# Performance work log

Hardware: AMD Instinct MI355X
Metric: run time of the kernel (lower is better)

The kernel has to match this reference:

```python
import jax, jax.numpy as jnp
import numpy as np

D_MODEL = 1024
NUM_HEADS = 16
D_HEAD = D_MODEL // NUM_HEADS
THETA = 10000.0
B, S = 2, 2048


def setup_inputs() -> dict:
    key = jax.random.key(0)
    ks = jax.random.split(key, 5)
    std = np.sqrt(2.0 / (D_MODEL + D_MODEL))
    x = jax.random.normal(ks[0], (B, S, D_MODEL), dtype=jnp.float32)
    Wq = jax.random.normal(ks[1], (D_MODEL, D_MODEL), dtype=jnp.float32) * std
    Wk = jax.random.normal(ks[2], (D_MODEL, D_MODEL), dtype=jnp.float32) * std
    Wv = jax.random.normal(ks[3], (D_MODEL, D_MODEL), dtype=jnp.float32) * std
    Wo = jax.random.normal(ks[4], (D_MODEL, D_MODEL), dtype=jnp.float32) * std
    token_positions = jnp.arange(S, dtype=jnp.int32)
    return {"x": x, "Wq": Wq, "Wk": Wk, "Wv": Wv, "Wo": Wo,
            "token_positions": token_positions}


def _apply_rope(t, token_positions):
    # t: [B, H, S, d_head]; interleaved (even/odd) RoPE
    dh = t.shape[-1]
    inv_freq = 1.0 / (THETA ** (jnp.arange(0, dh, 2, dtype=jnp.float32) / dh))
    freqs = token_positions.astype(jnp.float32)[:, None] * inv_freq  # [S, dh/2]
    cos = jnp.cos(freqs)  # broadcasts over B, H
    sin = jnp.sin(freqs)
    x1 = t[..., 0::2]
    x2 = t[..., 1::2]
    r1 = x1 * cos - x2 * sin
    r2 = x1 * sin + x2 * cos
    return jnp.stack([r1, r2], axis=-1).reshape(t.shape)


def reference(x, Wq, Wk, Wv, Wo, token_positions):
    b, s, d = x.shape
    h, dh = NUM_HEADS, D_HEAD

    def proj(W):
        y = x @ W.T  # [B, S, D]
        return y.reshape(b, s, h, dh).transpose(0, 2, 1, 3)  # [B, H, S, dh]

    q = _apply_rope(proj(Wq), token_positions)
    k = _apply_rope(proj(Wk), token_positions)
    v = proj(Wv)

    scores = jnp.einsum('bhqd,bhkd->bhqk', q, k) / jnp.sqrt(jnp.float32(dh))
    causal = jnp.tril(jnp.ones((s, s), dtype=bool))
    scores = jnp.where(causal, scores, jnp.float32(-jnp.inf))
    attn = jax.nn.softmax(scores, axis=-1)
    out = jnp.einsum('bhqk,bhkd->bhqd', attn, v)  # [B, H, S, dh]
    out = out.transpose(0, 2, 1, 3).reshape(b, s, d)
    return out @ Wo.T
```

## Files before the change

### kernel.cpp

```cpp
#include <hip/hip_runtime.h>
#include <hip/hip_bf16.h>
#include <math.h>

#define DMODEL 1024
#define NHEAD  16
#define DHEAD  64
#define BATCH  2
#define SEQ    2048
#define MROWS  (BATCH * SEQ)

typedef __attribute__((ext_vector_type(8))) __bf16 bf16x8;
typedef __attribute__((ext_vector_type(4))) float  f32x4;

__device__ __forceinline__ void load16_lds(const ushort* g, ushort* l) {
    __builtin_amdgcn_global_load_lds(
        (const __attribute__((address_space(1))) unsigned int*)g,
        (__attribute__((address_space(3))) unsigned int*)l, 16, 0, 0);
}

__device__ __forceinline__ ushort bf16u(float v) {
    __hip_bfloat16 h = __float2bfloat16(v);
    return *reinterpret_cast<ushort*>(&h);
}

__global__ __launch_bounds__(256)
void cast_f32_bf16(const float* __restrict__ s, ushort* __restrict__ d, int n) {
    const int i = (blockIdx.x * 256 + threadIdx.x) * 8;
    if (i >= n) return;
    const f32x4 a = *reinterpret_cast<const f32x4*>(s + i);
    const f32x4 b = *reinterpret_cast<const f32x4*>(s + i + 4);
    bf16x8 o;
    #pragma unroll
    for (int j = 0; j < 4; j++) { o[j] = (__bf16)a[j]; o[4 + j] = (__bf16)b[j]; }
    *reinterpret_cast<bf16x8*>(d + i) = o;
}

__global__ __launch_bounds__(256)
void cast_w4(const float* __restrict__ w0, const float* __restrict__ w1,
             const float* __restrict__ w2, const float* __restrict__ w3,
             ushort* __restrict__ dst) {
    const float* src = (blockIdx.y == 0) ? w0 : (blockIdx.y == 1) ? w1
                     : (blockIdx.y == 2) ? w2 : w3;
    const int i = (blockIdx.x * 256 + threadIdx.x) * 8;
    const f32x4 a = *reinterpret_cast<const f32x4*>(src + i);
    const f32x4 b = *reinterpret_cast<const f32x4*>(src + i + 4);
    bf16x8 o;
    #pragma unroll
    for (int j = 0; j < 4; j++) { o[j] = (__bf16)a[j]; o[4 + j] = (__bf16)b[j]; }
    *reinterpret_cast<bf16x8*>(dst + (size_t)blockIdx.y * DMODEL * DMODEL + i) = o;
}

__global__ __launch_bounds__(256)
void rope_tab(const int* __restrict__ pos, float2* __restrict__ tab) {
    const int idx = blockIdx.x * 256 + threadIdx.x;
    const int s = idx >> 5;
    const int i = idx & 31;
    const float p = (float)pos[s];
    const float inv = exp2f(-(float)i * 0.41524101186092f);
    float sn, cs;
    sincosf(p * inv, &sn, &cs);
    tab[idx] = make_float2(cs, sn);
}

#define QKV_BARRIER() do { asm volatile("" ::: "memory"); \
                           __builtin_amdgcn_s_barrier(); } while (0)

#define RD4(dst, p_)                                                          \
    _Pragma("unroll")                                                         \
    for (int rr_ = 0; rr_ < 4; rr_++)                                         \
        dst[rr_] = *reinterpret_cast<const bf16x8*>((p_) + rr_ * 512);

#define MFMA_G(AFR, BFR, IOFF)                                                \
    __builtin_amdgcn_s_setprio(1);                                            \
    _Pragma("unroll")                                                         \
    for (int im_ = 0; im_ < 4; im_++)                                         \
        _Pragma("unroll")                                                     \
        for (int jn_ = 0; jn_ < 4; jn_++)                                     \
            acc[(IOFF) + im_][jn_] = __builtin_amdgcn_mfma_f32_16x16x32_bf16( \
                AFR[im_], BFR[jn_], acc[(IOFF) + im_][jn_], 0, 0, 0);         \
    __builtin_amdgcn_s_setprio(0);

__global__ __launch_bounds__(512, 2)
void gemm_qkv(const ushort* __restrict__ A, const ushort* __restrict__ B,
              ushort* __restrict__ C, const float2* __restrict__ tab) {
    __shared__ __align__(16) ushort pool[65536];

    const int orig = blockIdx.y * gridDim.x + blockIdx.x;
    const int xcd  = orig & 7;
    const int ixd  = orig >> 3;
    const int by   = xcd * 2 + (ixd / 12);
    const int bx   = ixd % 12;
    const int m0   = by * 256;
    const int n0   = bx * 256;

    const int tid  = threadIdx.x;
    const int lane = tid & 63;
    const int w    = tid >> 6;
    const int l16  = lane & 15;
    const int quad = lane >> 4;
    const int wm   = (w >> 2) * 128;
    const int wn   = (w & 3) * 64;
    const int chq  = (quad ^ ((l16 & 3) ^ ((l16 & 4) >> 1))) << 3;
    const int srow = tid >> 2;
    const int ssc  = (tid & 3) ^ ((srow & 3) ^ ((srow & 4) >> 1));

    const ushort* gA = A + (size_t)(m0 + srow) * DMODEL + ssc * 8;
    const ushort* gB = B + (size_t)(n0 + srow) * DMODEL + ssc * 8;

    auto stageA = [&](int tt, int ks) {
        const int off = tt * 64 + ks * 32;
        const int lb  = ((tt & 1) << 15) + (ks << 13);
        load16_lds(gA + off,                &pool[lb + tid * 8]);
        load16_lds(gA + 128 * DMODEL + off, &pool[lb + 4096 + tid * 8]);
    };
    auto stageB = [&](int tt, int ks) {
        const int off = tt * 64 + ks * 32;
        const int lb  = ((tt & 1) << 15) + 16384 + (ks << 13);
        load16_lds(gB + off,                &pool[lb + tid * 8]);
        load16_lds(gB + 128 * DMODEL + off, &pool[lb + 4096 + tid * 8]);
    };

    stageA(0, 0); stageB(0, 0);
    stageA(0, 1); stageB(0, 1);
    stageA(1, 0); stageB(1, 0);

    f32x4 acc[8][4];
    #pragma unroll
    for (int i = 0; i < 8; i++)
        #pragma unroll
        for (int j = 0; j < 4; j++) acc[i][j] = (f32x4){0.f, 0.f, 0.f, 0.f};

    asm volatile("s_waitcnt vmcnt(4)" ::: "memory");
    __builtin_amdgcn_s_barrier();

    bf16x8 al[4], ah[4], bc[4], bn[4];

    { const ushort* p = pool + (wm + l16) * 32 + chq;           RD4(al, p); }
    { const ushort* q = pool + 16384 + (wn + l16) * 32 + chq;   RD4(bc, q); }

    #pragma unroll 1
    for (int t = 0; t < 16; t++) {
        const int buf  = (t & 1) << 15;
        const int bufn = buf ^ 32768;
        if (t <= 14) { stageA(t + 1, 1); stageB(t + 1, 1); }
        { const ushort* p = pool + buf + (wm + 64 + l16) * 32 + chq;
          RD4(ah, p); }
        MFMA_G(al, bc, 0);
        { const ushort* p = pool + buf + 8192 + (wm + l16) * 32 + chq;
          RD4(al, p);
          const ushort* q = pool + buf + 16384 + 8192 + (wn + l16) * 32 + chq;
          RD4(bn, q); }
        MFMA_G(ah, bc, 4);
        if (t <= 14) { asm volatile("s_waitcnt vmcnt(4)" ::: "memory"); }
        QKV_BARRIER();
        if (t <= 13) { stageA(t + 2, 0); stageB(t + 2, 0); }
        { const ushort* p = pool + buf + 8192 + (wm + 64 + l16) * 32 + chq;
          RD4(ah, p); }
        MFMA_G(al, bn, 0);
        if (t <= 14) {
            const ushort* p = pool + bufn + (wm + l16) * 32 + chq;
            RD4(al, p);
            const ushort* q = pool + bufn + 16384 + (wn + l16) * 32 + chq;
            RD4(bc, q);
        }
        MFMA_G(ah, bn, 4);
        if (t <= 13)      { asm volatile("s_waitcnt vmcnt(4)" ::: "memory"); }
        else if (t == 14) { asm volatile("s_waitcnt vmcnt(0)" ::: "memory"); }
        QKV_BARRIER();
    }

    const int nbase  = n0 + wn;
    const int tensor = nbase >> 10;
    const int hh     = (nbase & 1023) >> 6;
    if (tensor < 2) {
        ushort* Dt = C + (size_t)tensor * ((size_t)MROWS * DMODEL);
        #pragma unroll
        for (int i = 0; i < 8; i++)
            #pragma unroll
            for (int r = 0; r < 4; r++) {
                const int m  = m0 + wm + i * 16 + quad * 4 + r;
                const int bb = m >> 11;
                const int ss = m & (SEQ - 1);
                const float2* trow = tab + ss * 32;
                #pragma unroll
                for (int j = 0; j < 4; j++) {
                    const int f = j * 16 + l16;
                    const float2 cs = trow[f >> 1];
                    const float val = acc[i][j][r];
                    const float prt = __shfl_xor(val, 1, 64);
                    const float out = (f & 1) ? (prt * cs.y + val * cs.x)
                                              : (val * cs.x - prt * cs.y);
                    Dt[(((size_t)(bb * NHEAD + hh)) * SEQ + ss) * DHEAD + f] =
                        bf16u(out);
                }
            }
    } else {
        ushort* Tw = pool + w * 8192;
        #pragma unroll
        for (int i = 0; i < 8; i++)
            #pragma unroll
            for (int j = 0; j < 4; j++) {
                const int f  = j * 16 + l16;
                const int sx = (f & 7) << 3;
                #pragma unroll
                for (int r = 0; r < 4; r += 2) {
                    const int ml = i * 16 + quad * 4 + r;
                    ushort2 pk;
                    pk.x = bf16u(acc[i][j][r]);
                    pk.y = bf16u(acc[i][j][r + 1]);
                    *reinterpret_cast<ushort2*>(&Tw[f * 128 + (ml ^ sx)]) = pk;
                }
            }
        asm volatile("s_waitcnt lgkmcnt(0)" ::: "memory");
        ushort* Dv = C + 2 * ((size_t)MROWS * DMODEL);
        const int c  = lane & 15;
        const int fb = lane >> 4;
        #pragma unroll
        for (int rr = 0; rr < 16; rr++) {
            const int fl = rr * 4 + fb;
            const uint4 v = *reinterpret_cast<const uint4*>(
                &Tw[fl * 128 + ((c << 3) ^ ((fl & 7) << 3))]);
            *reinterpret_cast<uint4*>(
                &Dv[(size_t)(hh * 64 + fl) * MROWS + m0 + wm + (c << 3)]) = v;
        }
    }
}

__global__ __launch_bounds__(256)
void gemm_out64(const ushort* __restrict__ A, const ushort* __restrict__ B,
                float* __restrict__ C) {
    __shared__ __align__(16) ushort pool[12288];
    ushort* As = pool;
    ushort* Bs = pool + 4096;
    const int tid  = threadIdx.x;
    const int m0   = blockIdx.y * 64;
    const int n0   = blockIdx.x * 128;
    const int lane = tid & 63;
    const int w    = tid >> 6;
    const int l16  = lane & 15;
    const int quad = lane >> 4;
    const int wm   = (w >> 1) * 32;
    const int wn   = (w & 1) * 64;
    const int srow = tid >> 2;
    const int scol = (tid & 3) * 8;

    const int am  = m0 + srow;
    const int abb = am >> 11;
    const int ass = am & (SEQ - 1);
    const size_t abase = ((size_t)(abb * NHEAD)) * SEQ * DHEAD + (size_t)ass * DHEAD;

    f32x4 acc[2][4];
    #pragma unroll
    for (int i = 0; i < 2; i++)
        #pragma unroll
        for (int j = 0; j < 4; j++) acc[i][j] = (f32x4){0.f, 0.f, 0.f, 0.f};

    {
        const int h = scol >> 6, dh = scol & 63;
        load16_lds(A + abase + (size_t)h * SEQ * DHEAD + dh, &As[srow * 32 + scol]);
        #pragma unroll
        for (int half = 0; half < 2; half++) {
            const int row = srow + half * 64;
            load16_lds(B + (size_t)(n0 + row) * DMODEL + scol, &Bs[row * 32 + scol]);
        }
    }

    for (int t = 0; t < 32; t++) {
        const int bf = t & 1;
        __syncthreads();
        if (t + 1 < 32) {
            const int k0 = (t + 1) * 32;
            const int kk = k0 + scol;
            const int h = kk >> 6, dh = kk & 63;
            load16_lds(A + abase + (size_t)h * SEQ * DHEAD + dh,
                       &As[(bf ^ 1) * 2048 + srow * 32 + scol]);
            #pragma unroll
            for (int half = 0; half < 2; half++) {
                const int row = srow + half * 64;
                load16_lds(B + (size_t)(n0 + row) * DMODEL + k0 + scol,
                           &Bs[(bf ^ 1) * 4096 + row * 32 + scol]);
            }
        }
        const int oa = bf * 2048, ob_ = bf * 4096;
        bf16x8 af[2], bfr[4];
        #pragma unroll
        for (int s = 0; s < 2; s++)
            af[s] = *reinterpret_cast<const bf16x8*>(
                &As[oa + (wm + s * 16 + l16) * 32 + quad * 8]);
        #pragma unroll
        for (int s = 0; s < 4; s++)
            bfr[s] = *reinterpret_cast<const bf16x8*>(
                &Bs[ob_ + (wn + s * 16 + l16) * 32 + quad * 8]);
        #pragma unroll
        for (int i = 0; i < 2; i++)
            #pragma unroll
            for (int j = 0; j < 4; j++)
                acc[i][j] = __builtin_amdgcn_mfma_f32_16x16x32_bf16(
                    af[i], bfr[j], acc[i][j], 0, 0, 0);
    }
    #pragma unroll
    for (int i = 0; i < 2; i++)
        #pragma unroll
        for (int r = 0; r < 4; r++) {
            const int m = m0 + wm + i * 16 + quad * 4 + r;
            #pragma unroll
            for (int j = 0; j < 4; j++)
                C[(size_t)m * DMODEL + n0 + wn + j * 16 + l16] = acc[i][j][r];
        }
}

__global__ __launch_bounds__(256)
void attn_mfma6(const ushort* __restrict__ qb, const ushort* __restrict__ kb,
                const ushort* __restrict__ vtg, ushort* __restrict__ ob) {
    __shared__ __align__(16) ushort Ks[2][4096];
    __shared__ __align__(16) ushort Vs[2][4096];
    __shared__ ushort Pb[4][16][72];

    const int bh   = blockIdx.x;
    const int b    = bh >> 4;
    const int h    = bh & 15;
    const int qt   = (gridDim.y - 1) - blockIdx.y;
    const int tid  = threadIdx.x;
    const int w    = tid >> 6;
    const int lane = tid & 63;
    const int l16  = lane & 15;
    const int quad = lane >> 4;
    const size_t base = (size_t)bh * SEQ * DHEAD;

    const int qlo = qt * 64 + w * 16;

    const float SC = 0.125f * 1.44269504088896f;
    bf16x8 qa[2];
    {
        const size_t qo = base + (size_t)(qlo + l16) * DHEAD + quad * 8;
        qa[0] = *reinterpret_cast<const bf16x8*>(qb + qo);
        qa[1] = *reinterpret_cast<const bf16x8*>(qb + qo + 32);
        #pragma unroll
        for (int j = 0; j < 8; j++) {
            qa[0][j] = (__bf16)(SC * (float)qa[0][j]);
            qa[1][j] = (__bf16)(SC * (float)qa[1][j]);
        }
    }

    f32x4 oacc[4];
    #pragma unroll
    for (int s = 0; s < 4; s++) oacc[s] = (f32x4){0.f, 0.f, 0.f, 0.f};
    float l_ = 0.f;

    const int c0 = tid,        r0 = c0 >> 3, g0 = (c0 & 7) ^ (r0 & 7);
    const int c1 = 256 + tid,  r1 = c1 >> 3, g1 = (c1 & 7) ^ (r1 & 7);
    const ushort* kg0 = kb + base + (size_t)r0 * DHEAD + g0 * 8;
    const ushort* kg1 = kb + base + (size_t)r1 * DHEAD + g1 * 8;
    const ushort* vg0 = vtg + (size_t)(h * DHEAD + r0) * MROWS + b * SEQ + g0 * 8;
    const ushort* vg1 = vtg + (size_t)(h * DHEAD + r1) * MROWS + b * SEQ + g1 * 8;

    int koff[2][4];
    #pragma unroll
    for (int half = 0; half < 2; half++)
        #pragma unroll
        for (int sub = 0; sub < 4; sub++)
            koff[half][sub] = (sub * 16 + l16) * 64 +
                              (((half * 4 + quad) ^ (l16 & 7)) * 8);

    load16_lds(kg0, &Ks[0][c0 * 8]);
    load16_lds(kg1, &Ks[0][c1 * 8]);
    load16_lds(vg0, &Vs[0][c0 * 8]);
    load16_lds(vg1, &Vs[0][c1 * 8]);

    const int T = qt + 1;
    for (int t = 0; t < T; t++) {
        const int bf = t & 1;
        __syncthreads();
        if (t + 1 < T) {
            const size_t ko = (size_t)(t + 1) * 64 * DHEAD;
            const int    vo = (t + 1) * 64;
            load16_lds(kg0 + ko, &Ks[bf ^ 1][c0 * 8]);
            load16_lds(kg1 + ko, &Ks[bf ^ 1][c1 * 8]);
            load16_lds(vg0 + vo, &Vs[bf ^ 1][c0 * 8]);
            load16_lds(vg1 + vo, &Vs[bf ^ 1][c1 * 8]);
        }

        const bool diag = (t == qt);
        const int nsub = diag ? (w + 1) : 4;
        const int nhv  = diag ? ((w >> 1) + 1) : 2;

        f32x4 sacc[4];
        #pragma unroll
        for (int s = 0; s < 4; s++) sacc[s] = (f32x4){0.f, 0.f, 0.f, 0.f};
        #pragma unroll
        for (int half = 0; half < 2; half++)
            #pragma unroll
            for (int sub = 0; sub < 4; sub++)
                if (sub < nsub) {
                    const bf16x8 kf = *reinterpret_cast<const bf16x8*>(
                        &Ks[bf][koff[half][sub]]);
                    sacc[sub] = __builtin_amdgcn_mfma_f32_16x16x32_bf16(
                        kf, qa[half], sacc[sub], 0, 0, 0);
                }

        float ev[4][4];
        if (diag) {
            const int thr = qlo + l16 - t * 64;
            #pragma unroll
            for (int sub = 0; sub < 4; sub++)
                #pragma unroll
                for (int r = 0; r < 4; r++) {
                    const float e = (sub * 16 + quad * 4 + r <= thr)
                                        ? exp2f(sacc[sub][r]) : 0.f;
                    ev[sub][r] = e;
                    l_ += e;
                }
        } else {
            #pragma unroll
            for (int sub = 0; sub < 4; sub++)
                #pragma unroll
                for (int r = 0; r < 4; r++) {
                    const float e = exp2f(sacc[sub][r]);
                    ev[sub][r] = e;
                    l_ += e;
                }
        }

        #pragma unroll
        for (int sub = 0; sub < 4; sub++) {
            ushort4 pk;
            pk.x = bf16u(ev[sub][0]); pk.y = bf16u(ev[sub][1]);
            pk.z = bf16u(ev[sub][2]); pk.w = bf16u(ev[sub][3]);
            *reinterpret_cast<ushort4*>(&Pb[w][l16][sub * 16 + quad * 4]) = pk;
        }
        bf16x8 pa[2];
        pa[0] = *reinterpret_cast<const bf16x8*>(&Pb[w][l16][quad * 8]);
        pa[1] = *reinterpret_cast<const bf16x8*>(&Pb[w][l16][32 + quad * 8]);

        #pragma unroll
        for (int hk = 0; hk < 2; hk++) {
            if (hk >= nhv) break;
            #pragma unroll
            for (int sf = 0; sf < 4; sf++) {
                const bf16x8 vf = *reinterpret_cast<const bf16x8*>(
                    &Vs[bf][koff[hk][sf]]);
                oacc[sf] = __builtin_amdgcn_mfma_f32_16x16x32_bf16(
                    pa[hk], vf, oacc[sf], 0, 0, 0);
            }
        }
    }

    l_ += __shfl_xor(l_, 16, 64);
    l_ += __shfl_xor(l_, 32, 64);
    float inv[4];
    #pragma unroll
    for (int r = 0; r < 4; r++) inv[r] = 1.f / __shfl(l_, quad * 4 + r, 64);
    #pragma unroll
    for (int sub = 0; sub < 4; sub++)
        #pragma unroll
        for (int r = 0; r < 4; r++) {
            const int q = qlo + quad * 4 + r;
            ob[base + (size_t)q * DHEAD + sub * 16 + l16] =
                bf16u(oacc[sub][r] * inv[r]);
        }
}

extern "C" void kernel_launch(void* const* d_in, const int* in_sizes, int n_in,
                              void* d_out, int out_size, void* d_ws, size_t ws_size,
                              hipStream_t stream) {
    const float* x  = (const float*)d_in[0];
    const float* Wq = (const float*)d_in[1];
    const float* Wk = (const float*)d_in[2];
    const float* Wv = (const float*)d_in[3];
    const float* Wo = (const float*)d_in[4];
    const int* pos = (const int*)d_in[5];

    const size_t TEN = (size_t)MROWS * DMODEL;
    const size_t WEL = (size_t)DMODEL * DMODEL;
    ushort* xb   = (ushort*)d_ws;
    ushort* Wqkv = xb + TEN;
    ushort* Wob  = Wqkv + 3 * WEL;
    ushort* qb   = Wob + WEL;
    ushort* kb   = qb + TEN;
    ushort* vtb  = kb + TEN;
    ushort* ob   = vtb + TEN;
    float2* tab  = (float2*)(ob + TEN);

    dim3 blk(256);
    rope_tab<<<(SEQ * 32) / 256, blk, 0, stream>>>(pos, tab);
    cast_f32_bf16<<<TEN / (8 * 256), blk, 0, stream>>>(x, xb, (int)TEN);
    dim3 gcw(WEL / (8 * 256), 4);
    cast_w4<<<gcw, blk, 0, stream>>>(Wq, Wk, Wv, Wo, Wqkv);

    dim3 gqkv(3 * DMODEL / 256, MROWS / 256);
    gemm_qkv<<<gqkv, dim3(512), 0, stream>>>(xb, Wqkv, qb, tab);

    dim3 gattn(BATCH * NHEAD, SEQ / 64);
    attn_mfma6<<<gattn, blk, 0, stream>>>(qb, kb, vtb, ob);

    dim3 gout(DMODEL / 128, MROWS / 64);
    gemm_out64<<<gout, blk, 0, stream>>>(ob, Wob, (float*)d_out);
}
```

Before: 181.5 us.

## Merge cast kernels and rewrite output GEMM with 128x128 tiles and pipelining

Result: faster. 177.9 us (-2.0%).

```diff
diff --git a/kernel.cpp b/kernel.cpp
--- a/kernel.cpp
+++ b/kernel.cpp
@@ -24,30 +24,29 @@
 }
 
 __global__ __launch_bounds__(256)
-void cast_f32_bf16(const float* __restrict__ s, ushort* __restrict__ d, int n) {
-    const int i = (blockIdx.x * 256 + threadIdx.x) * 8;
-    if (i >= n) return;
-    const f32x4 a = *reinterpret_cast<const f32x4*>(s + i);
-    const f32x4 b = *reinterpret_cast<const f32x4*>(s + i + 4);
+void cast_all(const float* __restrict__ x,  const float* __restrict__ w0,
+              const float* __restrict__ w1, const float* __restrict__ w2,
+              const float* __restrict__ w3, ushort* __restrict__ xb,
+              ushort* __restrict__ wb) {
+    const int idx = (blockIdx.x * 256 + threadIdx.x) * 8;
+    const int TEN_ = MROWS * DMODEL;
+    const float* src;
+    ushort* dst;
+    if (idx < TEN_) {
+        src = x + idx;  dst = xb + idx;
+    } else {
+        const int r   = idx - TEN_;
+        const int sel = r >> 20;
+        const int off = r & (DMODEL * DMODEL - 1);
+        src = (sel == 0 ? w0 : sel == 1 ? w1 : sel == 2 ? w2 : w3) + off;
+        dst = wb + r;
+    }
+    const f32x4 a = *reinterpret_cast<const f32x4*>(src);
+    const f32x4 b = *reinterpret_cast<const f32x4*>(src + 4);
     bf16x8 o;
     #pragma unroll
     for (int j = 0; j < 4; j++) { o[j] = (__bf16)a[j]; o[4 + j] = (__bf16)b[j]; }
-    *reinterpret_cast<bf16x8*>(d + i) = o;
-}
-
-__global__ __launch_bounds__(256)
-void cast_w4(const float* __restrict__ w0, const float* __restrict__ w1,
-             const float* __restrict__ w2, const float* __restrict__ w3,
-             ushort* __restrict__ dst) {
-    const float* src = (blockIdx.y == 0) ? w0 : (blockIdx.y == 1) ? w1
-                     : (blockIdx.y == 2) ? w2 : w3;
-    const int i = (blockIdx.x * 256 + threadIdx.x) * 8;
-    const f32x4 a = *reinterpret_cast<const f32x4*>(src + i);
-    const f32x4 b = *reinterpret_cast<const f32x4*>(src + i + 4);
-    bf16x8 o;
-    #pragma unroll
-    for (int j = 0; j < 4; j++) { o[j] = (__bf16)a[j]; o[4 + j] = (__bf16)b[j]; }
-    *reinterpret_cast<bf16x8*>(dst + (size_t)blockIdx.y * DMODEL * DMODEL + i) = o;
+    *reinterpret_cast<bf16x8*>(dst) = o;
 }
 
 __global__ __launch_bounds__(256)
@@ -226,85 +225,113 @@
     }
 }
 
-__global__ __launch_bounds__(256)
-void gemm_out64(const ushort* __restrict__ A, const ushort* __restrict__ B,
-                float* __restrict__ C) {
-    __shared__ __align__(16) ushort pool[12288];
-    ushort* As = pool;
-    ushort* Bs = pool + 4096;
+#define RD2(dst, p_)                                                          \
+    _Pragma("unroll")                                                         \
+    for (int rr_ = 0; rr_ < 2; rr_++)                                         \
+        dst[rr_] = *reinterpret_cast<const bf16x8*>((p_) + rr_ * 512);
+
+#define OUT_MFMA_G(AFR, BFR, IOFF)                                            \
+    __builtin_amdgcn_s_setprio(1);                                            \
+    _Pragma("unroll")                                                         \
+    for (int im_ = 0; im_ < 2; im_++)                                         \
+        _Pragma("unroll")                                                     \
+        for (int jn_ = 0; jn_ < 2; jn_++)                                     \
+            acc[(IOFF) + im_][jn_] = __builtin_amdgcn_mfma_f32_16x16x32_bf16( \
+                AFR[im_], BFR[jn_], acc[(IOFF) + im_][jn_], 0, 0, 0);         \
+    __builtin_amdgcn_s_setprio(0);
+
+__global__ __launch_bounds__(512, 2)
+void gemm_out128(const ushort* __restrict__ A, const ushort* __restrict__ B,
+                 float* __restrict__ C) {
+    __shared__ __align__(16) ushort pool[32768];
+
+    const int orig = blockIdx.y * gridDim.x + blockIdx.x;
+    const int n0   = (orig & 7) * 128;
+    const int m0   = (orig >> 3) * 128;
+
     const int tid  = threadIdx.x;
-    const int m0   = blockIdx.y * 64;
-    const int n0   = blockIdx.x * 128;
     const int lane = tid & 63;
     const int w    = tid >> 6;
     const int l16  = lane & 15;
     const int quad = lane >> 4;
-    const int wm   = (w >> 1) * 32;
-    const int wn   = (w & 1) * 64;
+    const int wm   = (w >> 2) * 64;
+    const int wn   = (w & 3) * 32;
+    const int chq  = (quad ^ ((l16 & 3) ^ ((l16 & 4) >> 1))) << 3;
     const int srow = tid >> 2;
-    const int scol = (tid & 3) * 8;
+    const int ssc  = (tid & 3) ^ ((srow & 3) ^ ((srow & 4) >> 1));
 
     const int am  = m0 + srow;
     const int abb = am >> 11;
     const int ass = am & (SEQ - 1);
-    const size_t abase = ((size_t)(abb * NHEAD)) * SEQ * DHEAD + (size_t)ass * DHEAD;
-
-    f32x4 acc[2][4];
-    #pragma unroll
-    for (int i = 0; i < 2; i++)
-        #pragma unroll
-        for (int j = 0; j < 4; j++) acc[i][j] = (f32x4){0.f, 0.f, 0.f, 0.f};
-
-    {
-        const int h = scol >> 6, dh = scol & 63;
-        load16_lds(A + abase + (size_t)h * SEQ * DHEAD + dh, &As[srow * 32 + scol]);
-        #pragma unroll
-        for (int half = 0; half < 2; half++) {
-            const int row = srow + half * 64;
-            load16_lds(B + (size_t)(n0 + row) * DMODEL + scol, &Bs[row * 32 + scol]);
-        }
+    const ushort* gA = A + ((size_t)(abb * NHEAD)) * SEQ * DHEAD
+                         + (size_t)ass * DHEAD + ssc * 8;
+    const ushort* gB = B + (size_t)(n0 + srow) * DMODEL + ssc * 8;
+
+    auto stageA = [&](int tt, int ks) {
+        load16_lds(gA + tt * (SEQ * DHEAD) + ks * 32,
+                   &pool[((tt & 1) << 14) + (ks << 12) + tid * 8]);
+    };
+    auto stageB = [&](int tt, int ks) {
+        load16_lds(gB + tt * 64 + ks * 32,
+                   &pool[((tt & 1) << 14) + 8192 + (ks << 12) + tid * 8]);
+    };
+
+    stageA(0, 0); stageB(0, 0);
+    stageA(0, 1); stageB(0, 1);
+    stageA(1, 0); stageB(1, 0);
+
+    f32x4 acc[4][2];
+    #pragma unroll
+    for (int i = 0; i < 4; i++)
+        #pragma unroll
+        for (int j = 0; j < 2; j++) acc[i][j] = (f32x4){0.f, 0.f, 0.f, 0.f};
+
+    asm volatile("s_waitcnt vmcnt(2)" ::: "memory");
+    __builtin_amdgcn_s_barrier();
+
+    bf16x8 al[2], ah[2], bc[2], bn[2];
+
+    { const ushort* p = pool + (wm + l16) * 32 + chq;          RD2(al, p); }
+    { const ushort* q = pool + 8192 + (wn + l16) * 32 + chq;   RD2(bc, q); }
+
+    #pragma unroll 1
+    for (int t = 0; t < 16; t++) {
+        const int buf  = (t & 1) << 14;
+        const int bufn = buf ^ 16384;
+        if (t <= 14) { stageA(t + 1, 1); stageB(t + 1, 1); }
+        { const ushort* p = pool + buf + (wm + 32 + l16) * 32 + chq;
+          RD2(ah, p); }
+        OUT_MFMA_G(al, bc, 0);
+        { const ushort* p = pool + buf + 4096 + (wm + l16) * 32 + chq;
+          RD2(al, p);
+          const ushort* q = pool + buf + 8192 + 4096 + (wn + l16) * 32 + chq;
+          RD2(bn, q); }
+        OUT_MFMA_G(ah, bc, 2);
+        if (t <= 14) { asm volatile("s_waitcnt vmcnt(2)" ::: "memory"); }
+        QKV_BARRIER();
+        if (t <= 13) { stageA(t + 2, 0); stageB(t + 2, 0); }
+        { const ushort* p = pool + buf + 4096 + (wm + 32 + l16) * 32 + chq;
+          RD2(ah, p); }
+        OUT_MFMA_G(al, bn, 0);
+        if (t <= 14) {
+            const ushort* p = pool + bufn + (wm + l16) * 32 + chq;
+            RD2(al, p);
+            const ushort* q = pool + bufn + 8192 + (wn + l16) * 32 + chq;
+            RD2(bc, q);
+        }
+        OUT_MFMA_G(ah, bn, 2);
+        if (t <= 13)      { asm volatile("s_waitcnt vmcnt(2)" ::: "memory"); }
+        else if (t == 14) { asm volatile("s_waitcnt vmcnt(0)" ::: "memory"); }
+        QKV_BARRIER();
     }
 
-    for (int t = 0; t < 32; t++) {
-        const int bf = t & 1;
-        __syncthreads();
-        if (t + 1 < 32) {
-            const int k0 = (t + 1) * 32;
-            const int kk = k0 + scol;
-            const int h = kk >> 6, dh = kk & 63;
-            load16_lds(A + abase + (size_t)h * SEQ * DHEAD + dh,
-                       &As[(bf ^ 1) * 2048 + srow * 32 + scol]);
-            #pragma unroll
-            for (int half = 0; half < 2; half++) {
-                const int row = srow + half * 64;
-                load16_lds(B + (size_t)(n0 + row) * DMODEL + k0 + scol,
-                           &Bs[(bf ^ 1) * 4096 + row * 32 + scol]);
-            }
-        }
-        const int oa = bf * 2048, ob_ = bf * 4096;
-        bf16x8 af[2], bfr[4];
-        #pragma unroll
-        for (int s = 0; s < 2; s++)
-            af[s] = *reinterpret_cast<const bf16x8*>(
-                &As[oa + (wm + s * 16 + l16) * 32 + quad * 8]);
-        #pragma unroll
-        for (int s = 0; s < 4; s++)
-            bfr[s] = *reinterpret_cast<const bf16x8*>(
-                &Bs[ob_ + (wn + s * 16 + l16) * 32 + quad * 8]);
-        #pragma unroll
-        for (int i = 0; i < 2; i++)
-            #pragma unroll
-            for (int j = 0; j < 4; j++)
-                acc[i][j] = __builtin_amdgcn_mfma_f32_16x16x32_bf16(
-                    af[i], bfr[j], acc[i][j], 0, 0, 0);
-    }
-    #pragma unroll
-    for (int i = 0; i < 2; i++)
+    #pragma unroll
+    for (int i = 0; i < 4; i++)
         #pragma unroll
         for (int r = 0; r < 4; r++) {
             const int m = m0 + wm + i * 16 + quad * 4 + r;
             #pragma unroll
-            for (int j = 0; j < 4; j++)
+            for (int j = 0; j < 2; j++)
                 C[(size_t)m * DMODEL + n0 + wn + j * 16 + l16] = acc[i][j][r];
         }
 }
@@ -483,9 +510,8 @@
 
     dim3 blk(256);
     rope_tab<<<(SEQ * 32) / 256, blk, 0, stream>>>(pos, tab);
-    cast_f32_bf16<<<TEN / (8 * 256), blk, 0, stream>>>(x, xb, (int)TEN);
-    dim3 gcw(WEL / (8 * 256), 4);
-    cast_w4<<<gcw, blk, 0, stream>>>(Wq, Wk, Wv, Wo, Wqkv);
+    cast_all<<<(TEN + 4 * WEL) / (8 * 256), blk, 0, stream>>>(
+        x, Wq, Wk, Wv, Wo, xb, Wqkv);
 
     dim3 gqkv(3 * DMODEL / 256, MROWS / 256);
     gemm_qkv<<<gqkv, dim3(512), 0, stream>>>(xb, Wqkv, qb, tab);
@@ -493,6 +519,6 @@
     dim3 gattn(BATCH * NHEAD, SEQ / 64);
     attn_mfma6<<<gattn, blk, 0, stream>>>(qb, kb, vtb, ob);
 
-    dim3 gout(DMODEL / 128, MROWS / 64);
-    gemm_out64<<<gout, blk, 0, stream>>>(ob, Wob, (float*)d_out);
-}
+    dim3 gout(DMODEL / 128, MROWS / 128);
+    gemm_out128<<<gout, dim3(512), 0, stream>>>(ob, Wob, (float*)d_out);
+}
```
